# Kernel tuning notes

Hardware: AMD Instinct MI355X
Metric: run time of the kernel (lower is better)

## Reference

```python
import jax, jax.numpy as jnp
import numpy as np

B, L, D, E = 32, 2048, 1024, 2048

def setup_inputs() -> dict:
    key = jax.random.key(0)
    k1, k2, k3, k4, k5 = jax.random.split(key, 5)
    scale_s = 1.0 / np.sqrt(D)
    scale_h = 1.0 / np.sqrt(E)
    return {
        "dec_hidden": jax.random.normal(k1, (B, D), jnp.float32),
        "enc_outputs": jax.random.normal(k2, (B, L, E), jnp.float32),
        "W_s": jax.random.normal(k3, (D, D), jnp.float32) * scale_s,
        "W_h": jax.random.normal(k4, (D, E), jnp.float32) * scale_h,
        "v": jax.random.normal(k5, (D,), jnp.float32) * scale_s,
    }

def reference(dec_hidden, enc_outputs, W_s, W_h, v):
    # s: [B, D] -- projected decoder state (broadcast over src_len, no repeat)
    s = jnp.einsum('bd,ed->be', dec_hidden, W_s)
    # h: [B, L, D] -- projected encoder outputs
    h = jnp.einsum('ble,de->bld', enc_outputs, W_h)
    # additive scores: v^T tanh(s + h) -> [B, L]
    scores = jnp.einsum('bld,d->bl', jnp.tanh(s[:, None, :] + h), v)
    attn = jax.nn.softmax(scores, axis=1)
    # context: weighted sum of encoder outputs -> [B, E]
    ctx = jnp.einsum('bl,ble->be', attn, enc_outputs)
    return (ctx, attn)
```

## Files before the change

kernel.cpp:

```cpp
#include <hip/hip_runtime.h>
#include <cstdint>
#include <cstddef>

#define B_ 32
#define L_ 2048
#define D_ 1024
#define E_ 2048

typedef __attribute__((ext_vector_type(8))) short short8;
typedef __attribute__((ext_vector_type(16))) float f32x16;
typedef __attribute__((ext_vector_type(4))) unsigned int uint4v;

__device__ __forceinline__ unsigned int pack_bf16_2(float lo, float hi) {
  unsigned int ul = __builtin_bit_cast(unsigned int, lo) + 0x8000u;
  unsigned int uh = __builtin_bit_cast(unsigned int, hi) + 0x8000u;
  return (ul >> 16) | (uh & 0xFFFF0000u);
}

__device__ __forceinline__ unsigned int cvt_pk_bf16(float lo, float hi) {
  unsigned int r;
  asm("v_cvt_pk_bf16_f32 %0, %1, %2" : "=v"(r) : "v"(lo), "v"(hi));
  return r;
}

__device__ __forceinline__ float fast_tanh(float x) {
  float e = __expf(2.0f * x);
  return 1.0f - 2.0f / (e + 1.0f);
}

__global__ __launch_bounds__(256) void k_s(const float* __restrict__ dec,
                                           const float* __restrict__ Ws,
                                           float* __restrict__ s) {
  int wid = threadIdx.x >> 6, lane = threadIdx.x & 63;
  int out = blockIdx.x * 4 + wid;
  int b = out >> 10, i = out & 1023;
  const float* dr = dec + b * D_;
  const float* wr = Ws + (size_t)i * D_;
  float acc = 0.f;
#pragma unroll
  for (int c = 0; c < 4; ++c) {
    int d0 = c * 256 + lane * 4;
    float4 x = *(const float4*)(dr + d0);
    float4 w = *(const float4*)(wr + d0);
    acc += x.x * w.x + x.y * w.y + x.z * w.z + x.w * w.w;
  }
#pragma unroll
  for (int off = 32; off >= 1; off >>= 1) acc += __shfl_xor(acc, off, 64);
  if (lane == 0) s[out] = acc;
}

__global__ __launch_bounds__(256) void k_cvt(const float* __restrict__ src,
                                             unsigned short* __restrict__ dst) {
  size_t i = ((size_t)blockIdx.x * 256 + threadIdx.x) * 8;
  float4 a = *(const float4*)(src + i);
  float4 b = *(const float4*)(src + i + 4);
  uint4v p;
  p.x = pack_bf16_2(a.x, a.y);
  p.y = pack_bf16_2(a.z, a.w);
  p.z = pack_bf16_2(b.x, b.y);
  p.w = pack_bf16_2(b.z, b.w);
  *(uint4v*)(dst + i) = p;
}

__global__ __launch_bounds__(256, 2) void k_gemm(const float* __restrict__ enc,
                                                 const unsigned short* __restrict__ whb,
                                                 const float* __restrict__ sbias,
                                                 const float* __restrict__ vvec,
                                                 float* __restrict__ scores) {
  __shared__ alignas(16) unsigned short As[64 * 128];
  __shared__ alignas(16) unsigned short Bs[64 * 128];

  const int tid = threadIdx.x;
  const int wid = tid >> 6;
  const int lane = tid & 63;
  const int wm = wid >> 1;
  const int wn = wid & 1;

  const int flat = blockIdx.x;
  const int nt = (flat >> 3) & 7;
  const int mt = (flat & 7) | ((flat >> 6) << 3);
  const int m_base = mt * 128, n_base = nt * 128;
  const int b_idx = m_base >> 11;

  const int aRow = lane >> 4;
  const int aG = lane & 15;
  const float* gAr = enc + (size_t)(m_base + wid * 32 + aRow) * E_ + aG * 4;
  const int aUl = (aRow & 1) * 8 + (aG >> 1);
  const int aBy = (aG & 1) * 8;
  int aWoff[8];
#pragma unroll
  for (int i = 0; i < 8; ++i) {
    int line = wid * 16 + i * 2 + (aRow >> 1);
    aWoff[i] = line * 256 + ((aUl ^ (line & 15)) << 4) + aBy;
  }

  const int rp = lane >> 4;
  const int u0 = (lane & 15) ^ rp;
  const unsigned short* gB = whb + (size_t)n_base * E_;
  int offB[4], ldsB[4];
#pragma unroll
  for (int it = 0; it < 4; ++it) {
    int ulog = u0 ^ (it << 2);
    offB[it] = (wid * 32 + it * 8 + 2 * rp + (ulog >> 3)) * E_ + (ulog & 7) * 8;
    ldsB[it] = (wid * 16 + it * 4) * 256 + lane * 16;
  }

  const int col = lane & 31;
  const int h = lane >> 5;
  int soff[4];
#pragma unroll
  for (int ks = 0; ks < 4; ++ks)
    soff[ks] = ((((col & 1) << 3) + ks * 2 + h) ^ ((col >> 1) & 15)) << 4;
  const char* aBase[2];
#pragma unroll
  for (int mi = 0; mi < 2; ++mi)
    aBase[mi] = (const char*)As + (wm * 32 + mi * 16 + (col >> 1)) * 256;
  const char* bBase[2];
#pragma unroll
  for (int ni = 0; ni < 2; ++ni)
    bBase[ni] = (const char*)Bs + (wn * 32 + ni * 16 + (col >> 1)) * 256;

  f32x16 acc[2][2] = {};
  float4 rAv0[8], rAv1[8];
  uint4v rBv[4];

#pragma unroll
  for (int it = 0; it < 4; ++it)
    rBv[it] = *(const uint4v*)(gB + offB[it]);
#pragma unroll
  for (int i = 0; i < 8; ++i)
    rAv0[i] = *(const float4*)(gAr + (size_t)(i * 4) * E_);
#pragma unroll
  for (int i = 0; i < 8; ++i)
    rAv1[i] = *(const float4*)(gAr + (size_t)(i * 4) * E_ + 64);

#define GPHASE(KK, RA, DO_B, DO_A)                                          \
  {                                                                         \
    uint2 qa[8];                                                            \
    _Pragma("unroll") for (int i = 0; i < 8; ++i) {                         \
      qa[i].x = cvt_pk_bf16(RA[i].x, RA[i].y);                              \
      qa[i].y = cvt_pk_bf16(RA[i].z, RA[i].w);                              \
    }                                                                       \
    __builtin_amdgcn_sched_barrier(0);                                      \
    __builtin_amdgcn_s_barrier();         \
    __builtin_amdgcn_sched_barrier(0);                                      \
    _Pragma("unroll") for (int i = 0; i < 8; ++i)                           \
      *(uint2*)((char*)As + aWoff[i]) = qa[i];                              \
    _Pragma("unroll") for (int it = 0; it < 4; ++it)                        \
      *(uint4v*)((char*)Bs + ldsB[it]) = rBv[it];                           \
    if (DO_B) {                                                             \
      _Pragma("unroll") for (int it = 0; it < 4; ++it)                      \
        rBv[it] = *(const uint4v*)(gB + offB[it] + (KK) + 64);              \
    }                                                                       \
    if (DO_A) {                                                             \
      _Pragma("unroll") for (int i = 0; i < 8; ++i)                         \
        RA[i] = *(const float4*)(gAr + (size_t)(i * 4) * E_ + (KK) + 128);  \
    }                                                                       \
    asm volatile("s_waitcnt lgkmcnt(0)" ::: "memory");                      \
    __builtin_amdgcn_sched_barrier(0);                                      \
    __builtin_amdgcn_s_barrier();                    \
    __builtin_amdgcn_sched_barrier(0);                                      \
    _Pragma("unroll") for (int ks = 0; ks < 4; ++ks) {                      \
      short8 bf[2], af[2];                                                  \
      _Pragma("unroll") for (int ni = 0; ni < 2; ++ni)                      \
        bf[ni] = *(const short8*)(bBase[ni] + soff[ks]);                    \
      _Pragma("unroll") for (int mi = 0; mi < 2; ++mi)                      \
        af[mi] = *(const short8*)(aBase[mi] + soff[ks]);                    \
      _Pragma("unroll") for (int mi = 0; mi < 2; ++mi)                      \
        _Pragma("unroll") for (int ni = 0; ni < 2; ++ni)                    \
          acc[mi][ni] = __builtin_amdgcn_mfma_f32_32x32x16_bf16(            \
              af[mi], bf[ni], acc[mi][ni], 0, 0, 0);                        \
    }                                                                       \
  }

  for (int kk = 0; kk < 1920; kk += 128) {
    GPHASE(kk, rAv0, true, true);
    GPHASE(kk + 64, rAv1, true, true);
  }
  GPHASE(1920, rAv0, true, false);
  GPHASE(1984, rAv1, false, false);
#undef GPHASE

  float vv[2], sv[2];
#pragma unroll
  for (int ni = 0; ni < 2; ++ni) {
    int n = n_base + wn * 64 + ni * 32 + col;
    vv[ni] = vvec[n];
    sv[ni] = sbias[b_idx * D_ + n];
  }
#pragma unroll
  for (int mi = 0; mi < 2; ++mi) {
#pragma unroll
    for (int reg = 0; reg < 16; ++reg) {
      float sum = 0.f;
#pragma unroll
      for (int ni = 0; ni < 2; ++ni)
        sum += vv[ni] * fast_tanh(sv[ni] + acc[mi][ni][reg]);
      sum += __shfl_xor(sum, 1, 64);
      sum += __shfl_xor(sum, 2, 64);
      sum += __shfl_xor(sum, 4, 64);
      sum += __shfl_xor(sum, 8, 64);
      sum += __shfl_xor(sum, 16, 64);
      if (col == 0)
        atomicAdd(&scores[m_base + wm * 64 + mi * 32 + (reg & 3) + 8 * (reg >> 2) + h * 4], sum);
    }
  }
}

__global__ __launch_bounds__(256) void k_softmax(float* __restrict__ sc) {
  int b = blockIdx.x, tid = threadIdx.x;
  int lane = tid & 63, wid = tid >> 6;
  float* row = sc + (size_t)b * L_;
  float vals[8];
  float mx = -1e30f;
#pragma unroll
  for (int j = 0; j < 8; ++j) { vals[j] = row[tid + j * 256]; mx = fmaxf(mx, vals[j]); }
#pragma unroll
  for (int off = 32; off >= 1; off >>= 1) mx = fmaxf(mx, __shfl_xor(mx, off, 64));
  __shared__ float redm[4], reds[4];
  if (lane == 0) redm[wid] = mx;
  __syncthreads();
  mx = fmaxf(fmaxf(redm[0], redm[1]), fmaxf(redm[2], redm[3]));
  float sum = 0.f;
#pragma unroll
  for (int j = 0; j < 8; ++j) { vals[j] = __expf(vals[j] - mx); sum += vals[j]; }
#pragma unroll
  for (int off = 32; off >= 1; off >>= 1) sum += __shfl_xor(sum, off, 64);
  if (lane == 0) reds[wid] = sum;
  __syncthreads();
  sum = reds[0] + reds[1] + reds[2] + reds[3];
  float inv = 1.0f / sum;
#pragma unroll
  for (int j = 0; j < 8; ++j) row[tid + j * 256] = vals[j] * inv;
}

__global__ __launch_bounds__(256) void k_ctx(const float* __restrict__ enc,
                                             const float* __restrict__ attn,
                                             float* __restrict__ ctx) {
  int b = blockIdx.y;
  int lc = blockIdx.x >> 1;
  int eh = blockIdx.x & 1;
  int t = threadIdx.x;
  __shared__ float aw[64];
  if (t < 64) aw[t] = attn[(size_t)b * L_ + lc * 64 + t];
  __syncthreads();
  const float* base = enc + ((size_t)b * L_ + (size_t)lc * 64) * E_ + eh * 1024;
  float4 a0 = make_float4(0.f, 0.f, 0.f, 0.f);
#pragma unroll 8
  for (int l = 0; l < 64; ++l) {
    float w = aw[l];
    float4 x0 = *(const float4*)(base + (size_t)l * E_ + t * 4);
    a0.x += w * x0.x; a0.y += w * x0.y; a0.z += w * x0.z; a0.w += w * x0.w;
  }
  float* cb = ctx + (size_t)b * E_ + eh * 1024 + t * 4;
  atomicAdd(cb + 0, a0.x);
  atomicAdd(cb + 1, a0.y);
  atomicAdd(cb + 2, a0.z);
  atomicAdd(cb + 3, a0.w);
}

extern "C" void kernel_launch(void* const* d_in, const int* in_sizes, int n_in,
                              void* d_out, int out_size, void* d_ws, size_t ws_size,
                              hipStream_t stream) {
  const float* dec = (const float*)d_in[0];
  const float* enc = (const float*)d_in[1];
  const float* Ws  = (const float*)d_in[2];
  const float* Wh  = (const float*)d_in[3];
  const float* v   = (const float*)d_in[4];

  float* ctx  = (float*)d_out;
  float* attn = (float*)d_out + B_ * E_;

  unsigned short* whb = (unsigned short*)d_ws;
  float* sbuf = (float*)((char*)d_ws + (size_t)D_ * E_ * sizeof(unsigned short));

  hipMemsetAsync(d_out, 0, (size_t)out_size * sizeof(float), stream);

  k_s<<<dim3((B_ * D_) / 4), dim3(256), 0, stream>>>(dec, Ws, sbuf);
  k_cvt<<<dim3((D_ * E_) / (256 * 8)), dim3(256), 0, stream>>>(Wh, whb);
  k_gemm<<<dim3((B_ * L_ / 128) * (D_ / 128)), dim3(256), 0, stream>>>(enc, whb, sbuf, v, attn);
  k_softmax<<<dim3(B_), dim3(256), 0, stream>>>(attn);
  k_ctx<<<dim3(64, B_), dim3(256), 0, stream>>>(enc, attn, ctx);
}
```

Before: 1.069 ms.

## Double-buffer LDS in GEMM and replace ctx atomics with partial-sum reduction

The GEMM main loop now uses two LDS buffers for A and B. The next tile is written into the other buffer while MFMAs read the current one, which removes one of the two block barriers per k-step. The context kernel now has each block cover 128 rows instead of 64 and write per-chunk partial sums to the workspace, reusing the W_h bf16 buffer that is dead after the GEMM. A separate small kernel then reduces those partials, replacing the float atomics. LDS use per block doubles to 64KB, which could limit occupancy, and an extra kernel launch is added.

```diff
diff --git a/kernel.cpp b/kernel.cpp
--- a/kernel.cpp
+++ b/kernel.cpp
@@ -67,8 +67,8 @@
                                                  const float* __restrict__ sbias,
                                                  const float* __restrict__ vvec,
                                                  float* __restrict__ scores) {
-  __shared__ alignas(16) unsigned short As[64 * 128];
-  __shared__ alignas(16) unsigned short Bs[64 * 128];
+  __shared__ alignas(16) unsigned short As[2][64 * 128];
+  __shared__ alignas(16) unsigned short Bs[2][64 * 128];
 
   const int tid = threadIdx.x;
   const int wid = tid >> 6;
@@ -111,14 +111,11 @@
 #pragma unroll
   for (int ks = 0; ks < 4; ++ks)
     soff[ks] = ((((col & 1) << 3) + ks * 2 + h) ^ ((col >> 1) & 15)) << 4;
-  const char* aBase[2];
-#pragma unroll
-  for (int mi = 0; mi < 2; ++mi)
-    aBase[mi] = (const char*)As + (wm * 32 + mi * 16 + (col >> 1)) * 256;
-  const char* bBase[2];
-#pragma unroll
-  for (int ni = 0; ni < 2; ++ni)
-    bBase[ni] = (const char*)Bs + (wn * 32 + ni * 16 + (col >> 1)) * 256;
+  int aOff[2], bOff[2];
+#pragma unroll
+  for (int mi = 0; mi < 2; ++mi) aOff[mi] = (wm * 32 + mi * 16 + (col >> 1)) * 256;
+#pragma unroll
+  for (int ni = 0; ni < 2; ++ni) bOff[ni] = (wn * 32 + ni * 16 + (col >> 1)) * 256;
 
   f32x16 acc[2][2] = {};
   float4 rAv0[8], rAv1[8];
@@ -133,53 +130,78 @@
 #pragma unroll
   for (int i = 0; i < 8; ++i)
     rAv1[i] = *(const float4*)(gAr + (size_t)(i * 4) * E_ + 64);
-
-#define GPHASE(KK, RA, DO_B, DO_A)                                          \
+  {
+    uint2 qa[8];
+#pragma unroll
+    for (int i = 0; i < 8; ++i) {
+      qa[i].x = cvt_pk_bf16(rAv0[i].x, rAv0[i].y);
+      qa[i].y = cvt_pk_bf16(rAv0[i].z, rAv0[i].w);
+    }
+#pragma unroll
+    for (int i = 0; i < 8; ++i)
+      *(uint2*)((char*)As + aWoff[i]) = qa[i];
+#pragma unroll
+    for (int it = 0; it < 4; ++it)
+      *(uint4v*)((char*)Bs + ldsB[it]) = rBv[it];
+  }
+#pragma unroll
+  for (int it = 0; it < 4; ++it)
+    rBv[it] = *(const uint4v*)(gB + offB[it] + 64);
+#pragma unroll
+  for (int i = 0; i < 8; ++i)
+    rAv0[i] = *(const float4*)(gAr + (size_t)(i * 4) * E_ + 128);
+  asm volatile("s_waitcnt lgkmcnt(0)" ::: "memory");
+  __builtin_amdgcn_sched_barrier(0);
+  __builtin_amdgcn_s_barrier();
+  __builtin_amdgcn_sched_barrier(0);
+
+#define GSTEP(KK, RA, DO_PACK, DO_A, DO_B, RD)                              \
   {                                                                         \
-    uint2 qa[8];                                                            \
-    _Pragma("unroll") for (int i = 0; i < 8; ++i) {                         \
-      qa[i].x = cvt_pk_bf16(RA[i].x, RA[i].y);                              \
-      qa[i].y = cvt_pk_bf16(RA[i].z, RA[i].w);                              \
+    if (DO_PACK) {                                                          \
+      uint2 qa[8];                                                          \
+      _Pragma("unroll") for (int i = 0; i < 8; ++i) {                       \
+        qa[i].x = cvt_pk_bf16(RA[i].x, RA[i].y);                            \
+        qa[i].y = cvt_pk_bf16(RA[i].z, RA[i].w);                            \
+      }                                                                     \
+      _Pragma("unroll") for (int i = 0; i < 8; ++i)                         \
+        *(uint2*)((char*)As + ((RD) ^ 16384) + aWoff[i]) = qa[i];           \
+      _Pragma("unroll") for (int it = 0; it < 4; ++it)                      \
+        *(uint4v*)((char*)Bs + ((RD) ^ 16384) + ldsB[it]) = rBv[it];        \
     }                                                                       \
-    __builtin_amdgcn_sched_barrier(0);                                      \
-    __builtin_amdgcn_s_barrier();         \
-    __builtin_amdgcn_sched_barrier(0);                                      \
-    _Pragma("unroll") for (int i = 0; i < 8; ++i)                           \
-      *(uint2*)((char*)As + aWoff[i]) = qa[i];                              \
-    _Pragma("unroll") for (int it = 0; it < 4; ++it)                        \
-      *(uint4v*)((char*)Bs + ldsB[it]) = rBv[it];                           \
     if (DO_B) {                                                             \
       _Pragma("unroll") for (int it = 0; it < 4; ++it)                      \
-        rBv[it] = *(const uint4v*)(gB + offB[it] + (KK) + 64);              \
+        rBv[it] = *(const uint4v*)(gB + offB[it] + (KK) + 128);             \
     }                                                                       \
     if (DO_A) {                                                             \
       _Pragma("unroll") for (int i = 0; i < 8; ++i)                         \
-        RA[i] = *(const float4*)(gAr + (size_t)(i * 4) * E_ + (KK) + 128);  \
+        RA[i] = *(const float4*)(gAr + (size_t)(i * 4) * E_ + (KK) + 192);  \
     }                                                                       \
-    asm volatile("s_waitcnt lgkmcnt(0)" ::: "memory");                      \
-    __builtin_amdgcn_sched_barrier(0);                                      \
-    __builtin_amdgcn_s_barrier();                    \
-    __builtin_amdgcn_sched_barrier(0);                                      \
     _Pragma("unroll") for (int ks = 0; ks < 4; ++ks) {                      \
       short8 bf[2], af[2];                                                  \
       _Pragma("unroll") for (int ni = 0; ni < 2; ++ni)                      \
-        bf[ni] = *(const short8*)(bBase[ni] + soff[ks]);                    \
+        bf[ni] = *(const short8*)((char*)Bs + (RD) + bOff[ni] + soff[ks]);  \
       _Pragma("unroll") for (int mi = 0; mi < 2; ++mi)                      \
-        af[mi] = *(const short8*)(aBase[mi] + soff[ks]);                    \
+        af[mi] = *(const short8*)((char*)As + (RD) + aOff[mi] + soff[ks]);  \
       _Pragma("unroll") for (int mi = 0; mi < 2; ++mi)                      \
         _Pragma("unroll") for (int ni = 0; ni < 2; ++ni)                    \
           acc[mi][ni] = __builtin_amdgcn_mfma_f32_32x32x16_bf16(            \
               af[mi], bf[ni], acc[mi][ni], 0, 0, 0);                        \
     }                                                                       \
-  }
-
-  for (int kk = 0; kk < 1920; kk += 128) {
-    GPHASE(kk, rAv0, true, true);
-    GPHASE(kk + 64, rAv1, true, true);
-  }
-  GPHASE(1920, rAv0, true, false);
-  GPHASE(1984, rAv1, false, false);
-#undef GPHASE
+    asm volatile("s_waitcnt lgkmcnt(0)" ::: "memory");                      \
+    __builtin_amdgcn_sched_barrier(0);                                      \
+    __builtin_amdgcn_s_barrier();                                           \
+    __builtin_amdgcn_sched_barrier(0);                                      \
+  }
+
+  for (int kk = 0; kk < 1792; kk += 128) {
+    GSTEP(kk, rAv1, 1, 1, 1, 0);
+    GSTEP(kk + 64, rAv0, 1, 1, 1, 16384);
+  }
+  GSTEP(1792, rAv1, 1, 1, 1, 0);
+  GSTEP(1856, rAv0, 1, 0, 1, 16384);
+  GSTEP(1920, rAv1, 1, 0, 0, 0);
+  GSTEP(1984, rAv0, 0, 0, 0, 16384);
+#undef GSTEP
 
   float vv[2], sv[2];
 #pragma unroll
@@ -234,29 +256,39 @@
   for (int j = 0; j < 8; ++j) row[tid + j * 256] = vals[j] * inv;
 }
 
-__global__ __launch_bounds__(256) void k_ctx(const float* __restrict__ enc,
-                                             const float* __restrict__ attn,
-                                             float* __restrict__ ctx) {
+__global__ __launch_bounds__(256) void k_ctx_p(const float* __restrict__ enc,
+                                               const float* __restrict__ attn,
+                                               float* __restrict__ partial) {
   int b = blockIdx.y;
   int lc = blockIdx.x >> 1;
   int eh = blockIdx.x & 1;
   int t = threadIdx.x;
-  __shared__ float aw[64];
-  if (t < 64) aw[t] = attn[(size_t)b * L_ + lc * 64 + t];
+  __shared__ float aw[128];
+  if (t < 128) aw[t] = attn[(size_t)b * L_ + lc * 128 + t];
   __syncthreads();
-  const float* base = enc + ((size_t)b * L_ + (size_t)lc * 64) * E_ + eh * 1024;
+  const float* base = enc + ((size_t)b * L_ + (size_t)lc * 128) * E_ + eh * 1024;
   float4 a0 = make_float4(0.f, 0.f, 0.f, 0.f);
 #pragma unroll 8
-  for (int l = 0; l < 64; ++l) {
+  for (int l = 0; l < 128; ++l) {
     float w = aw[l];
     float4 x0 = *(const float4*)(base + (size_t)l * E_ + t * 4);
     a0.x += w * x0.x; a0.y += w * x0.y; a0.z += w * x0.z; a0.w += w * x0.w;
   }
-  float* cb = ctx + (size_t)b * E_ + eh * 1024 + t * 4;
-  atomicAdd(cb + 0, a0.x);
-  atomicAdd(cb + 1, a0.y);
-  atomicAdd(cb + 2, a0.z);
-  atomicAdd(cb + 3, a0.w);
+  *(float4*)(partial + ((size_t)(lc * 32 + b) * E_) + eh * 1024 + t * 4) = a0;
+}
+
+__global__ __launch_bounds__(256) void k_ctx_r(const float* __restrict__ partial,
+                                               float* __restrict__ ctx) {
+  int idx = blockIdx.x * 256 + threadIdx.x;
+  int b = idx >> 9;
+  int e4 = idx & 511;
+  float4 s = make_float4(0.f, 0.f, 0.f, 0.f);
+#pragma unroll
+  for (int c = 0; c < 16; ++c) {
+    float4 p = *(const float4*)(partial + ((size_t)(c * 32 + b) * E_) + e4 * 4);
+    s.x += p.x; s.y += p.y; s.z += p.z; s.w += p.w;
+  }
+  *(float4*)(ctx + (size_t)b * E_ + e4 * 4) = s;
 }
 
 extern "C" void kernel_launch(void* const* d_in, const int* in_sizes, int n_in,
@@ -272,6 +304,7 @@
   float* attn = (float*)d_out + B_ * E_;
 
   unsigned short* whb = (unsigned short*)d_ws;
+  float* partial = (float*)d_ws;
   float* sbuf = (float*)((char*)d_ws + (size_t)D_ * E_ * sizeof(unsigned short));
 
   hipMemsetAsync(d_out, 0, (size_t)out_size * sizeof(float), stream);
@@ -280,5 +313,6 @@
   k_cvt<<<dim3((D_ * E_) / (256 * 8)), dim3(256), 0, stream>>>(Wh, whb);
   k_gemm<<<dim3((B_ * L_ / 128) * (D_ / 128)), dim3(256), 0, stream>>>(enc, whb, sbuf, v, attn);
   k_softmax<<<dim3(B_), dim3(256), 0, stream>>>(attn);
-  k_ctx<<<dim3(64, B_), dim3(256), 0, stream>>>(enc, attn, ctx);
-}
+  k_ctx_p<<<dim3(32, B_), dim3(256), 0, stream>>>(enc, attn, partial);
+  k_ctx_r<<<dim3((B_ * E_) / (256 * 4)), dim3(256), 0, stream>>>(partial, ctx);
+}
```

Measured after the change: 1.065 ms. No clear change (-0.4%).
